# Kernel optimization log

Measured on AMD Instinct MI355X. Metric: run time of the kernel, lower is better.

Reference implementation:

```python
import jax, jax.numpy as jnp
import numpy as np

N, L, V = 8192, 50, 50000   # sentences, max words/sentence, vocab
D, H, O = 300, 150, 64      # embed dim, SAGE hidden, SAGE out
THRESH = 0.7
NEG = -1e9


def _sage_pool(h, A, mask, W1s, W1n, b1, W2s, W2n, b2, gw, gb):
    """Two-layer mean-aggregator SAGEConv + GlobalAttentionPooling, vectorized
    over N independent per-sentence graphs.
    h:[N,L,din] node feats, A:[N,L,L] bool adjacency (src u -> dst v), mask:[N,L] valid nodes."""
    Af = A.astype(h.dtype)
    deg = jnp.maximum(Af.sum(axis=1), 1.0)  # in-degree per dst node [N,L]

    def conv(x, Ws, Wn, b):
        m = jnp.einsum('nuv,nud->nvd', Af, x) / deg[..., None]  # mean of in-neighbors
        return x @ Ws + m @ Wn + b  # fc_self(x) + fc_neigh(mean)

    h1 = jax.nn.relu(conv(h, W1s, W1n, b1))
    h2 = conv(h1, W2s, W2n, b2)
    # global attention pooling: softmax(gate) over real nodes of each graph
    gate = jnp.squeeze(h2 @ gw, -1) + gb  # [N,L]
    attn = jax.nn.softmax(jnp.where(mask, gate, NEG), axis=-1)
    return jnp.einsum('nl,nld->nd', attn, h2)  # [N,O]


def setup_inputs() -> dict:
    key = jax.random.key(0)
    ks = jax.random.split(key, 32)
    pos = jnp.arange(L)
    lengths = jax.random.randint(ks[0], (N,), 5, L + 1)
    valid = pos[None, :] < lengths[:, None]  # [N,L] real-word mask (0 = pad)
    words = jax.random.randint(ks[1], (N, L), 1, V) * valid
    syntax_words = jax.random.randint(ks[2], (N, L), 1, V) * valid
    adj = jax.random.uniform(ks[3], (N, L, L)) < 0.08
    syntax_adj = (adj & valid[:, :, None] & valid[:, None, :]).astype(jnp.int32)
    hsg_feature = jax.random.normal(ks[4], (N, O), jnp.float32)

    def lin(k, i, o):
        return jax.random.normal(k, (i, o), jnp.float32) / np.sqrt(i)

    inp = {
        'words': words.astype(jnp.int32),
        'syntax_words': syntax_words.astype(jnp.int32),
        'syntax_adj': syntax_adj,
        'hsg_feature': hsg_feature,
        'embed': jax.random.normal(ks[5], (V, D), jnp.float32) * 0.1,
        'sem_W1s': lin(ks[6], D, H), 'sem_W1n': lin(ks[7], D, H), 'sem_b1': jnp.zeros((H,), jnp.float32),
        'sem_W2s': lin(ks[8], H, O), 'sem_W2n': lin(ks[9], H, O), 'sem_b2': jnp.zeros((O,), jnp.float32),
        'sem_gw': lin(ks[10], O, 1), 'sem_gb': jnp.zeros((1,), jnp.float32),
        'syn_W1s': lin(ks[11], D, H), 'syn_W1n': lin(ks[12], D, H), 'syn_b1': jnp.zeros((H,), jnp.float32),
        'syn_W2s': lin(ks[13], H, O), 'syn_W2n': lin(ks[14], H, O), 'syn_b2': jnp.zeros((O,), jnp.float32),
        'syn_gw': lin(ks[15], O, 1), 'syn_gb': jnp.zeros((1,), jnp.float32),
        'cls_w1': lin(ks[16], 3 * O, 128), 'cls_b1': jnp.zeros((128,), jnp.float32),
        'cls_w2': lin(ks[17], 128, 2), 'cls_b2': jnp.zeros((2,), jnp.float32),
    }
    return inp


def reference(words, syntax_words, syntax_adj, hsg_feature, embed,
              sem_W1s, sem_W1n, sem_b1, sem_W2s, sem_W2n, sem_b2, sem_gw, sem_gb,
              syn_W1s, syn_W1n, syn_b1, syn_W2s, syn_W2n, syn_b2, syn_gw, syn_gb,
              cls_w1, cls_b1, cls_w2, cls_b2):
    # --- semantic graph: per-sentence cosine-similarity thresholding ---
    mask = words > 0
    emb = embed[words]  # [N,L,D] gather
    nrm = emb / jnp.maximum(jnp.linalg.norm(emb, axis=-1, keepdims=True), 1e-8)
    cos = jnp.einsum('nld,nmd->nlm', nrm, nrm)  # [N,L,L]
    semA = (cos > THRESH) & mask[:, :, None] & mask[:, None, :]  # includes self-loops (cos=1)
    sem_feat = _sage_pool(emb, semA, mask,
                          sem_W1s, sem_W1n, sem_b1, sem_W2s, sem_W2n, sem_b2, sem_gw, sem_gb)
    # --- syntax graph: given per-sentence adjacency over its word ids ---
    syn_mask = syntax_words > 0
    syn_emb = embed[syntax_words]
    syn_feat = _sage_pool(syn_emb, syntax_adj.astype(bool), syn_mask,
                          syn_W1s, syn_W1n, syn_b1, syn_W2s, syn_W2n, syn_b2, syn_gw, syn_gb)
    # --- concat with HSG sentence state, classify ---
    feat = jnp.concatenate([sem_feat, syn_feat, hsg_feature], axis=-1)  # [N,192]
    hid = jax.nn.relu(feat @ cls_w1 + cls_b1)
    return hid @ cls_w2 + cls_b2  # [N,2]
```

## Files before the change

kernel.cpp:

```cpp
#include <hip/hip_runtime.h>

#define NS 8192
#define L  50

typedef unsigned short u16;
typedef unsigned int   u32;
typedef __attribute__((ext_vector_type(8))) __bf16 bf16x8;
typedef __attribute__((ext_vector_type(4))) float  f32x4;

#define OFF_X    0
#define OFF_TT   0
#define OFF_T2T  0
#define OFF_ATTN 0
#define OFF_H1   21760
#define OFF_RED  21760
#define OFF_M    43264
#define OFF_DIAG 43264
#define OFF_WID  52480
#define OFF_CLO  52736
#define OFF_CHI  52992
#define OFF_RDEG 53248
#define SMEM_SZ  53504

#define XSTR  328
#define TSTR  68
#define H1STR 168
#define MSTR  72

#define W1_ROWS 320
#define W1_KP   328
#define W2_ROWS 128
#define W2_KP   168

__device__ __forceinline__ u16 f2bf(float f) {
  u32 u = __float_as_uint(f);
  u += 0x7fffu + ((u >> 16) & 1u);
  return (u16)(u >> 16);
}
__device__ __forceinline__ float bf2f(u16 h) {
  return __uint_as_float(((u32)h) << 16);
}
__device__ __forceinline__ f32x4 mfma16(bf16x8 a, bf16x8 b, f32x4 c) {
  return __builtin_amdgcn_mfma_f32_16x16x32_bf16(a, b, c, 0, 0, 0);
}
__device__ __forceinline__ uint2 pack4bf(f32x4 c) {
  uint2 p;
  p.x = (u32)f2bf(c[0]) | ((u32)f2bf(c[1]) << 16);
  p.y = (u32)f2bf(c[2]) | ((u32)f2bf(c[3]) << 16);
  return p;
}
union BF8U { bf16x8 v; uint4 u; };
__device__ __forceinline__ bf16x8 ld_bf8_b64pair(const u16* p) {
  uint2 a = *(const uint2*)p;
  uint2 b = *(const uint2*)(p + 4);
  BF8U r; r.u = make_uint4(a.x, a.y, b.x, b.y);
  return r.v;
}

struct GParams {
  const int* words; const int* syn_words; const int* syn_adj;
  const float* embed;
  const float* sem_b1; const float* sem_b2; const float* sem_gw; const float* sem_gb;
  const float* syn_b1; const float* syn_b2; const float* syn_gw; const float* syn_gb;
  const u16* w1t_sem; const u16* w1t_syn; const u16* w2t_sem; const u16* w2t_syn;
  float* semf; float* synf;
};

__global__ __launch_bounds__(256, 3) void sage_kernel(GParams P) {
  __shared__ __align__(16) char smem[SMEM_SZ];
  int*   wid   = (int*)(smem + OFF_WID);
  u32*   clo   = (u32*)(smem + OFF_CLO);
  u32*   chi   = (u32*)(smem + OFF_CHI);
  float* rdegp = (float*)(smem + OFF_RDEG);
  float* diag  = (float*)(smem + OFF_DIAG);

  const int tid  = threadIdx.x;
  const int lane = tid & 63;
  const int w    = tid >> 6;
  const int ln   = lane & 15;
  const int quad = lane >> 4;

  const bool semg = (blockIdx.x < NS);
  const int  n    = semg ? blockIdx.x : (blockIdx.x - NS);

  const int*   wsrc = semg ? P.words   : P.syn_words;
  const u16*   W1T  = semg ? P.w1t_sem : P.w1t_syn;
  const u16*   W2T  = semg ? P.w2t_sem : P.w2t_syn;
  const float* b1g  = semg ? P.sem_b1  : P.syn_b1;
  const float* b2g  = semg ? P.sem_b2  : P.syn_b2;
  const float* gw   = semg ? P.sem_gw  : P.syn_gw;
  const float* gb   = semg ? P.sem_gb  : P.syn_gb;
  float* featout    = semg ? P.semf    : P.synf;

  const int jts[3] = {w, w + 4, 8 + (w & 1)};

  if (tid < 64) {
    wid[tid] = (tid < L) ? wsrc[(size_t)n * L + tid] : 0;
    clo[tid] = 0u; chi[tid] = 0u;
  }
  __syncthreads();

  for (int i = 0; i < 16; ++i) {
    const int v = w + 4 * i;
    const int word = wid[v];
    const float* src = P.embed + (size_t)word * 300;
    u16* xrow = (u16*)(smem + OFF_X) + v * XSTR;
    for (int l = lane; l < 82; l += 64) {
      uint2 pk = make_uint2(0u, 0u);
      if (word > 0 && l < 75) {
        float4 f = *(const float4*)(src + l * 4);
        pk.x = (u32)f2bf(f.x) | ((u32)f2bf(f.y) << 16);
        pk.y = (u32)f2bf(f.z) | ((u32)f2bf(f.w) << 16);
      }
      *(uint2*)(xrow + l * 4) = pk;
    }
  }
  __syncthreads();

  if (semg) {
    const f32x4 z4 = {0.f, 0.f, 0.f, 0.f};
    f32x4 g[4] = {z4, z4, z4, z4};
    const char* xb = smem + OFF_X;
    const int arow = (w * 16 + ln) * (XSTR * 2) + quad * 16;
    for (int kk = 0; kk < 10; ++kk) {
      bf16x8 a = *(const bf16x8*)(xb + arow + kk * 64);
      #pragma unroll
      for (int nt = 0; nt < 4; ++nt) {
        bf16x8 b = *(const bf16x8*)(xb + (nt * 16 + ln) * (XSTR * 2) + quad * 16 + kk * 64);
        g[nt] = mfma16(a, b, g[nt]);
      }
    }
    {
      const int r = ln - quad * 4;
      if (r >= 0 && r < 4) {
        #pragma unroll
        for (int nt = 0; nt < 4; ++nt) {
          if (nt == w) {
            float val = (r == 0) ? g[nt][0] : (r == 1) ? g[nt][1]
                      : (r == 2) ? g[nt][2] : g[nt][3];
            diag[w * 16 + ln] = val;
          }
        }
      }
    }
    __syncthreads();
    if (tid < 64) { float dd = diag[tid]; diag[tid] = 1.0f / sqrtf(fmaxf(dd, 1e-12f)); }
    __syncthreads();
    {
      const int ubase = w * 16 + quad * 4;
      float ru[4]; int uok[4];
      #pragma unroll
      for (int r = 0; r < 4; ++r) { ru[r] = diag[ubase + r]; uok[r] = wid[ubase + r] > 0; }
      #pragma unroll
      for (int nt = 0; nt < 4; ++nt) {
        const int v = nt * 16 + ln;
        const float rv = diag[v];
        const bool vok = wid[v] > 0;
        u32 nib = 0u;
        #pragma unroll
        for (int r = 0; r < 4; ++r) {
          float c = g[nt][r] * ru[r] * rv;
          if (vok && uok[r] && c > 0.7f) nib |= (1u << r);
        }
        if (nib) {
          if (ubase < 32) atomicOr(&clo[v], nib << ubase);
          else            atomicOr(&chi[v], nib << (ubase - 32));
        }
      }
    }
  } else {
    const int* abase = P.syn_adj + (size_t)n * (L * L);
    for (int v = w; v < L; v += 4) {
      int val = (lane < L) ? abase[lane * L + v] : 0;
      unsigned long long m = __ballot(val != 0);
      if (lane == 0) { clo[v] = (u32)m; chi[v] = (u32)(m >> 32); }
    }
  }
  __syncthreads();

  if (tid < 64) {
    int dg = __popc(clo[tid]) + __popc(chi[tid]);
    rdegp[tid] = 1.0f / (float)(dg > 0 ? dg : 1);
  }
  {
    const int v = lane, half = w;
    const u32 src = (half < 2) ? clo[v] : chi[v];
    const int sh = (half & 1) * 16;
    u16* Mrow = (u16*)(smem + OFF_M) + v * MSTR + half * 16;
    #pragma unroll
    for (int c = 0; c < 4; ++c) {
      uint2 pk;
      u32 b0 = (src >> (sh + 4 * c + 0)) & 1u;
      u32 b1 = (src >> (sh + 4 * c + 1)) & 1u;
      u32 b2 = (src >> (sh + 4 * c + 2)) & 1u;
      u32 b3 = (src >> (sh + 4 * c + 3)) & 1u;
      pk.x = (b0 ? 0x3F80u : 0u) | (b1 ? 0x3F800000u : 0u);
      pk.y = (b2 ? 0x3F80u : 0u) | (b3 ? 0x3F800000u : 0u);
      *(uint2*)(Mrow + 4 * c) = pk;
    }
  }

  const f32x4 z4 = {0.f, 0.f, 0.f, 0.f};
  f32x4 tacc[3][4], sacc[3][4];
  #pragma unroll
  for (int i = 0; i < 3; ++i)
    #pragma unroll
    for (int m = 0; m < 4; ++m) { tacc[i][m] = z4; sacc[i][m] = z4; }
  {
    const char* xb = smem + OFF_X;
    for (int kk = 0; kk < 10; ++kk) {
      bf16x8 x[4];
      #pragma unroll
      for (int m = 0; m < 4; ++m)
        x[m] = *(const bf16x8*)(xb + (m * 16 + ln) * (XSTR * 2) + quad * 16 + kk * 64);
      bf16x8 bn[3], as[3];
      #pragma unroll
      for (int i = 0; i < 3; ++i) {
        const int jt = jts[i];
        bn[i] = *(const bf16x8*)(W1T + (size_t)(jt * 16 + ln) * W1_KP + kk * 32 + quad * 8);
        as[i] = *(const bf16x8*)(W1T + (size_t)((jt + 10) * 16 + ln) * W1_KP + kk * 32 + quad * 8);
      }
      #pragma unroll
      for (int i = 0; i < 3; ++i)
        #pragma unroll
        for (int m = 0; m < 4; ++m) {
          tacc[i][m] = mfma16(x[m], bn[i], tacc[i][m]);
          sacc[i][m] = mfma16(as[i], x[m], sacc[i][m]);
        }
    }
  }
  __syncthreads();

  {
    u16* tt = (u16*)(smem + OFF_TT);
    #pragma unroll
    for (int i = 0; i < 3; ++i) {
      const int jt = jts[i];
      #pragma unroll
      for (int m = 0; m < 4; ++m) {
        const int v0 = m * 16 + quad * 4;
        *(uint2*)(tt + (jt * 16 + ln) * TSTR + v0) = pack4bf(tacc[i][m]);
      }
    }
  }

  bf16x8 mb0[4], mb1[4];
  {
    const u16* Mp = (const u16*)(smem + OFF_M);
    #pragma unroll
    for (int vt = 0; vt < 4; ++vt) {
      mb0[vt] = *(const bf16x8*)(Mp + (vt * 16 + ln) * MSTR + quad * 8);
      mb1[vt] = *(const bf16x8*)(Mp + (vt * 16 + ln) * MSTR + quad * 8 + 32);
    }
  }
  float rd[4];
  #pragma unroll
  for (int vt = 0; vt < 4; ++vt) rd[vt] = rdegp[vt * 16 + ln];
  {
    const u16* tt = (const u16*)(smem + OFF_TT);
    u16* h1p = (u16*)(smem + OFF_H1);
    #pragma unroll
    for (int i = 0; i < 3; ++i) {
      const int jt = jts[i];
      f32x4 gacc[4] = {z4, z4, z4, z4};
      const u16* tb = tt + (jt * 16 + ln) * TSTR + quad * 8;
      bf16x8 ta0 = ld_bf8_b64pair(tb);
      bf16x8 ta1 = ld_bf8_b64pair(tb + 32);
      #pragma unroll
      for (int vt = 0; vt < 4; ++vt) {
        gacc[vt] = mfma16(ta0, mb0[vt], gacc[vt]);
        gacc[vt] = mfma16(ta1, mb1[vt], gacc[vt]);
      }
      const int j0 = jt * 16 + quad * 4;
      float bv[4];
      #pragma unroll
      for (int r = 0; r < 4; ++r) { int j = j0 + r; bv[r] = (j < 150) ? b1g[j] : 0.f; }
      #pragma unroll
      for (int vt = 0; vt < 4; ++vt) {
        const int v = vt * 16 + ln;
        f32x4 hv;
        #pragma unroll
        for (int r = 0; r < 4; ++r)
          hv[r] = fmaxf(sacc[i][vt][r] + gacc[vt][r] * rd[vt] + bv[r], 0.f);
        *(uint2*)(h1p + v * H1STR + j0) = pack4bf(hv);
      }
    }
  }
  __syncthreads();

  f32x4 s2acc[4] = {z4, z4, z4, z4};
  f32x4 h2v[4];
  {
    f32x4 t2acc[4] = {z4, z4, z4, z4};
    const u16* h1p = (const u16*)(smem + OFF_H1);
    for (int kk = 0; kk < 5; ++kk) {
      bf16x8 h[4];
      #pragma unroll
      for (int t4 = 0; t4 < 4; ++t4)
        h[t4] = *(const bf16x8*)(h1p + (t4 * 16 + ln) * H1STR + kk * 32 + quad * 8);
      bf16x8 a2  = *(const bf16x8*)(W2T + (size_t)(w * 16 + ln) * W2_KP + kk * 32 + quad * 8);
      bf16x8 b2f = *(const bf16x8*)(W2T + (size_t)((4 + w) * 16 + ln) * W2_KP + kk * 32 + quad * 8);
      #pragma unroll
      for (int vt = 0; vt < 4; ++vt) {
        s2acc[vt] = mfma16(a2, h[vt], s2acc[vt]);
        t2acc[vt] = mfma16(h[vt], b2f, t2acc[vt]);
      }
    }
    u16* t2t = (u16*)(smem + OFF_T2T);
    #pragma unroll
    for (int m = 0; m < 4; ++m) {
      const int v0 = m * 16 + quad * 4;
      *(uint2*)(t2t + (w * 16 + ln) * TSTR + v0) = pack4bf(t2acc[m]);
    }
    f32x4 g2[4] = {z4, z4, z4, z4};
    const u16* t2b = t2t + (w * 16 + ln) * TSTR + quad * 8;
    bf16x8 u0 = ld_bf8_b64pair(t2b);
    bf16x8 u1 = ld_bf8_b64pair(t2b + 32);
    #pragma unroll
    for (int vt = 0; vt < 4; ++vt) {
      g2[vt] = mfma16(u0, mb0[vt], g2[vt]);
      g2[vt] = mfma16(u1, mb1[vt], g2[vt]);
    }
    const int j0q = w * 16 + quad * 4;
    float b2v[4];
    #pragma unroll
    for (int r = 0; r < 4; ++r) b2v[r] = b2g[j0q + r];
    #pragma unroll
    for (int vt = 0; vt < 4; ++vt)
      #pragma unroll
      for (int r = 0; r < 4; ++r)
        h2v[vt][r] = s2acc[vt][r] + g2[vt][r] * rd[vt] + b2v[r];
  }
  __syncthreads();

  {
    const int j0q = w * 16 + quad * 4;
    float gwv[4];
    #pragma unroll
    for (int r = 0; r < 4; ++r) gwv[r] = gw[j0q + r];
    float* redp = (float*)(smem + OFF_RED);
    #pragma unroll
    for (int vt = 0; vt < 4; ++vt) {
      float p = h2v[vt][0] * gwv[0] + h2v[vt][1] * gwv[1]
              + h2v[vt][2] * gwv[2] + h2v[vt][3] * gwv[3];
      redp[(vt * 16 + ln) * 17 + (w * 4 + quad)] = p;
    }
  }
  __syncthreads();

  if (tid < 64) {
    const float* redp = (const float*)(smem + OFF_RED);
    float g = gb[0];
    #pragma unroll
    for (int i = 0; i < 16; ++i) g += redp[tid * 17 + i];
    const bool val = wid[tid] > 0;
    g = val ? g : -1e30f;
    float mx = g;
    #pragma unroll
    for (int off = 32; off; off >>= 1) mx = fmaxf(mx, __shfl_xor(mx, off));
    float e = val ? __expf(g - mx) : 0.f;
    float ssum = e;
    #pragma unroll
    for (int off = 32; off; off >>= 1) ssum += __shfl_xor(ssum, off);
    ((float*)(smem + OFF_ATTN))[tid] = e / ssum;
  }
  __syncthreads();

  {
    const float* attnp = (const float*)(smem + OFF_ATTN);
    float av[4];
    #pragma unroll
    for (int vt = 0; vt < 4; ++vt) av[vt] = attnp[vt * 16 + ln];
    float xr[4];
    #pragma unroll
    for (int r = 0; r < 4; ++r) {
      float x = av[0] * h2v[0][r] + av[1] * h2v[1][r]
              + av[2] * h2v[2][r] + av[3] * h2v[3][r];
      #pragma unroll
      for (int off = 1; off < 16; off <<= 1) x += __shfl_xor(x, off);
      xr[r] = x;
    }
    if (ln == 0) {
      const int j0q = w * 16 + quad * 4;
      *(float4*)(featout + (size_t)n * 64 + j0q) = make_float4(xr[0], xr[1], xr[2], xr[3]);
    }
  }
}

__global__ void prep_w1(const float* Wn, const float* Ws, u16* dst) {
  int idx = blockIdx.x * 256 + threadIdx.x;
  if (idx >= W1_ROWS * W1_KP) return;
  int nn = idx / W1_KP, k = idx - nn * W1_KP;
  float v = 0.f;
  if (k < 300) {
    if (nn < 150) v = Wn[k * 150 + nn];
    else if (nn >= 160 && nn < 310) v = Ws[k * 150 + (nn - 160)];
  }
  dst[idx] = f2bf(v);
}
__global__ void prep_w2(const float* Ws, const float* Wn, u16* dst) {
  int idx = blockIdx.x * 256 + threadIdx.x;
  if (idx >= W2_ROWS * W2_KP) return;
  int nn = idx / W2_KP, k = idx - nn * W2_KP;
  float v = 0.f;
  if (k < 150) v = (nn < 64) ? Ws[k * 64 + nn] : Wn[k * 64 + (nn - 64)];
  dst[idx] = f2bf(v);
}

__global__ __launch_bounds__(128) void cls_kernel(const float* semf, const float* synf,
                                                  const float* hsg,
                                                  const float* w1, const float* b1,
                                                  const float* w2, const float* b2,
                                                  float* out) {
  __shared__ float feat[32][192];
  __shared__ float hid[32][132];
  const int r0 = blockIdx.x * 32;
  for (int idx = threadIdx.x; idx < 32 * 192; idx += 128) {
    int r = idx / 192, c = idx % 192;
    float v;
    if (c < 64)        v = semf[(size_t)(r0 + r) * 64 + c];
    else if (c < 128)  v = synf[(size_t)(r0 + r) * 64 + (c - 64)];
    else               v = hsg [(size_t)(r0 + r) * 64 + (c - 128)];
    feat[r][c] = v;
  }
  __syncthreads();
  {
    const int j = threadIdx.x;
    float acc[32];
    float bb = b1[j];
    #pragma unroll
    for (int r = 0; r < 32; ++r) acc[r] = bb;
    for (int k = 0; k < 192; ++k) {
      float ww = w1[(size_t)k * 128 + j];
      #pragma unroll
      for (int r = 0; r < 32; ++r) acc[r] += feat[r][k] * ww;
    }
    #pragma unroll
    for (int r = 0; r < 32; ++r) hid[r][j] = fmaxf(acc[r], 0.0f);
  }
  __syncthreads();
  if (threadIdx.x < 64) {
    const int r = threadIdx.x >> 1, o = threadIdx.x & 1;
    float a = b2[o];
    for (int h = 0; h < 128; ++h) a += hid[r][h] * w2[h * 2 + o];
    out[(size_t)(r0 + r) * 2 + o] = a;
  }
}

extern "C" void kernel_launch(void* const* d_in, const int* in_sizes, int n_in,
                              void* d_out, int out_size, void* d_ws, size_t ws_size,
                              hipStream_t stream) {
  GParams P;
  P.words     = (const int*)d_in[0];
  P.syn_words = (const int*)d_in[1];
  P.syn_adj   = (const int*)d_in[2];
  const float* hsg = (const float*)d_in[3];
  P.embed   = (const float*)d_in[4];
  const float* sem_W1s = (const float*)d_in[5];
  const float* sem_W1n = (const float*)d_in[6];
  P.sem_b1  = (const float*)d_in[7];
  const float* sem_W2s = (const float*)d_in[8];
  const float* sem_W2n = (const float*)d_in[9];
  P.sem_b2  = (const float*)d_in[10];
  P.sem_gw  = (const float*)d_in[11];
  P.sem_gb  = (const float*)d_in[12];
  const float* syn_W1s = (const float*)d_in[13];
  const float* syn_W1n = (const float*)d_in[14];
  P.syn_b1  = (const float*)d_in[15];
  const float* syn_W2s = (const float*)d_in[16];
  const float* syn_W2n = (const float*)d_in[17];
  P.syn_b2  = (const float*)d_in[18];
  P.syn_gw  = (const float*)d_in[19];
  P.syn_gb  = (const float*)d_in[20];
  const float* cls_w1 = (const float*)d_in[21];
  const float* cls_b1 = (const float*)d_in[22];
  const float* cls_w2 = (const float*)d_in[23];
  const float* cls_b2 = (const float*)d_in[24];

  float* semf = (float*)d_ws;
  float* synf = semf + (size_t)NS * 64;
  u16* w1t_sem = (u16*)((char*)d_ws + (size_t)4 * 1024 * 1024);
  u16* w1t_syn = w1t_sem + W1_ROWS * W1_KP;
  u16* w2t_sem = w1t_syn + W1_ROWS * W1_KP;
  u16* w2t_syn = w2t_sem + W2_ROWS * W2_KP;
  P.semf = semf; P.synf = synf;
  P.w1t_sem = w1t_sem; P.w1t_syn = w1t_syn;
  P.w2t_sem = w2t_sem; P.w2t_syn = w2t_syn;

  const int g1 = (W1_ROWS * W1_KP + 255) / 256;
  const int g2 = (W2_ROWS * W2_KP + 255) / 256;
  prep_w1<<<g1, 256, 0, stream>>>(sem_W1n, sem_W1s, w1t_sem);
  prep_w1<<<g1, 256, 0, stream>>>(syn_W1n, syn_W1s, w1t_syn);
  prep_w2<<<g2, 256, 0, stream>>>(sem_W2s, sem_W2n, w2t_sem);
  prep_w2<<<g2, 256, 0, stream>>>(syn_W2s, syn_W2n, w2t_syn);

  sage_kernel<<<2 * NS, 256, 0, stream>>>(P);
  cls_kernel<<<NS / 32, 128, 0, stream>>>(semf, synf, hsg, cls_w1, cls_b1,
                                          cls_w2, cls_b2, (float*)d_out);
}
```

Before: 882.9 us.

## Rebalance layer-1 MFMA work across waves, interleave graph blocks, cheaper bf16 conversion

Several changes at once. Layer-1 output tiles are redistributed so each wave holds 5 accumulator sets instead of 6, and the mask fragments are reloaded from LDS rather than held in registers, cutting register pressure. Semantic and syntax blocks are interleaved by block index. The syntax adjacency is read with coalesced int4 loads plus LDS atomics instead of strided ballots. The embedding bf16 conversion switches to round-half-up without ties-to-even, and the cosine Gram loop reuses B fragments as the A operand. It also adds a barrier before the layer-1 aggregation.

```diff
diff --git a/kernel.cpp b/kernel.cpp
--- a/kernel.cpp
+++ b/kernel.cpp
@@ -37,9 +37,6 @@
   u += 0x7fffu + ((u >> 16) & 1u);
   return (u16)(u >> 16);
 }
-__device__ __forceinline__ float bf2f(u16 h) {
-  return __uint_as_float(((u32)h) << 16);
-}
 __device__ __forceinline__ f32x4 mfma16(bf16x8 a, bf16x8 b, f32x4 c) {
   return __builtin_amdgcn_mfma_f32_16x16x32_bf16(a, b, c, 0, 0, 0);
 }
@@ -80,8 +77,8 @@
   const int ln   = lane & 15;
   const int quad = lane >> 4;
 
-  const bool semg = (blockIdx.x < NS);
-  const int  n    = semg ? blockIdx.x : (blockIdx.x - NS);
+  const bool semg = (blockIdx.x & 1) == 0;
+  const int  n    = blockIdx.x >> 1;
 
   const int*   wsrc = semg ? P.words   : P.syn_words;
   const u16*   W1T  = semg ? P.w1t_sem : P.w1t_syn;
@@ -91,8 +88,6 @@
   const float* gw   = semg ? P.sem_gw  : P.syn_gw;
   const float* gb   = semg ? P.sem_gb  : P.syn_gb;
   float* featout    = semg ? P.semf    : P.synf;
-
-  const int jts[3] = {w, w + 4, 8 + (w & 1)};
 
   if (tid < 64) {
     wid[tid] = (tid < L) ? wsrc[(size_t)n * L + tid] : 0;
@@ -109,8 +104,12 @@
       uint2 pk = make_uint2(0u, 0u);
       if (word > 0 && l < 75) {
         float4 f = *(const float4*)(src + l * 4);
-        pk.x = (u32)f2bf(f.x) | ((u32)f2bf(f.y) << 16);
-        pk.y = (u32)f2bf(f.z) | ((u32)f2bf(f.w) << 16);
+        u32 ax = __float_as_uint(f.x) + 0x8000u;
+        u32 ay = __float_as_uint(f.y) + 0x8000u;
+        u32 az = __float_as_uint(f.z) + 0x8000u;
+        u32 aw = __float_as_uint(f.w) + 0x8000u;
+        pk.x = (ax >> 16) | (ay & 0xffff0000u);
+        pk.y = (az >> 16) | (aw & 0xffff0000u);
       }
       *(uint2*)(xrow + l * 4) = pk;
     }
@@ -121,14 +120,14 @@
     const f32x4 z4 = {0.f, 0.f, 0.f, 0.f};
     f32x4 g[4] = {z4, z4, z4, z4};
     const char* xb = smem + OFF_X;
-    const int arow = (w * 16 + ln) * (XSTR * 2) + quad * 16;
     for (int kk = 0; kk < 10; ++kk) {
-      bf16x8 a = *(const bf16x8*)(xb + arow + kk * 64);
-      #pragma unroll
-      for (int nt = 0; nt < 4; ++nt) {
-        bf16x8 b = *(const bf16x8*)(xb + (nt * 16 + ln) * (XSTR * 2) + quad * 16 + kk * 64);
-        g[nt] = mfma16(a, b, g[nt]);
-      }
+      bf16x8 bfr[4];
+      #pragma unroll
+      for (int nt = 0; nt < 4; ++nt)
+        bfr[nt] = *(const bf16x8*)(xb + (nt * 16 + ln) * (XSTR * 2) + quad * 16 + kk * 64);
+      const bf16x8 a = bfr[w];
+      #pragma unroll
+      for (int nt = 0; nt < 4; ++nt) g[nt] = mfma16(a, bfr[nt], g[nt]);
     }
     {
       const int r = ln - quad * 4;
@@ -170,10 +169,23 @@
     }
   } else {
     const int* abase = P.syn_adj + (size_t)n * (L * L);
-    for (int v = w; v < L; v += 4) {
-      int val = (lane < L) ? abase[lane * L + v] : 0;
-      unsigned long long m = __ballot(val != 0);
-      if (lane == 0) { clo[v] = (u32)m; chi[v] = (u32)(m >> 32); }
+    const int4* a4 = (const int4*)abase;
+    for (int i = 0; i < 3; ++i) {
+      int idx4 = tid + 256 * i;
+      if (idx4 < 625) {
+        int4 a = a4[idx4];
+        int base = idx4 * 4;
+        const int av[4] = {a.x, a.y, a.z, a.w};
+        #pragma unroll
+        for (int e = 0; e < 4; ++e) {
+          if (av[e] != 0) {
+            int el = base + e;
+            int u = el / 50, v = el - u * 50;
+            if (u < 32) atomicOr(&clo[v], 1u << u);
+            else        atomicOr(&chi[v], 1u << (u - 32));
+          }
+        }
+      }
     }
   }
   __syncthreads();
@@ -201,32 +213,43 @@
   }
 
   const f32x4 z4 = {0.f, 0.f, 0.f, 0.f};
-  f32x4 tacc[3][4], sacc[3][4];
+  const int r0w = (w)      * 16 + ln;
+  const int r1w = (w + 4)  * 16 + ln;
+  const int r2w = ((w < 2) ? (w + 8) : (16 + w)) * 16 + ln;
+  const int r3w = (10 + w) * 16 + ln;
+  const int r4w = (14 + w) * 16 + ln;
+  f32x4 acc[5][4];
   #pragma unroll
-  for (int i = 0; i < 3; ++i)
-    #pragma unroll
-    for (int m = 0; m < 4; ++m) { tacc[i][m] = z4; sacc[i][m] = z4; }
+  for (int i = 0; i < 5; ++i)
+    #pragma unroll
+    for (int m = 0; m < 4; ++m) acc[i][m] = z4;
   {
     const char* xb = smem + OFF_X;
     for (int kk = 0; kk < 10; ++kk) {
+      const int wo = kk * 32 + quad * 8;
       bf16x8 x[4];
       #pragma unroll
       for (int m = 0; m < 4; ++m)
         x[m] = *(const bf16x8*)(xb + (m * 16 + ln) * (XSTR * 2) + quad * 16 + kk * 64);
-      bf16x8 bn[3], as[3];
-      #pragma unroll
-      for (int i = 0; i < 3; ++i) {
-        const int jt = jts[i];
-        bn[i] = *(const bf16x8*)(W1T + (size_t)(jt * 16 + ln) * W1_KP + kk * 32 + quad * 8);
-        as[i] = *(const bf16x8*)(W1T + (size_t)((jt + 10) * 16 + ln) * W1_KP + kk * 32 + quad * 8);
-      }
-      #pragma unroll
-      for (int i = 0; i < 3; ++i)
+      bf16x8 bf0 = *(const bf16x8*)(W1T + (size_t)r0w * W1_KP + wo);
+      bf16x8 bf1 = *(const bf16x8*)(W1T + (size_t)r1w * W1_KP + wo);
+      bf16x8 bf2 = *(const bf16x8*)(W1T + (size_t)r2w * W1_KP + wo);
+      bf16x8 bf3 = *(const bf16x8*)(W1T + (size_t)r3w * W1_KP + wo);
+      bf16x8 bf4 = *(const bf16x8*)(W1T + (size_t)r4w * W1_KP + wo);
+      #pragma unroll
+      for (int m = 0; m < 4; ++m) {
+        acc[0][m] = mfma16(x[m], bf0, acc[0][m]);
+        acc[1][m] = mfma16(x[m], bf1, acc[1][m]);
+        acc[3][m] = mfma16(bf3, x[m], acc[3][m]);
+        acc[4][m] = mfma16(bf4, x[m], acc[4][m]);
+      }
+      if (w < 2) {
         #pragma unroll
-        for (int m = 0; m < 4; ++m) {
-          tacc[i][m] = mfma16(x[m], bn[i], tacc[i][m]);
-          sacc[i][m] = mfma16(as[i], x[m], sacc[i][m]);
-        }
+        for (int m = 0; m < 4; ++m) acc[2][m] = mfma16(x[m], bf2, acc[2][m]);
+      } else {
+        #pragma unroll
+        for (int m = 0; m < 4; ++m) acc[2][m] = mfma16(bf2, x[m], acc[2][m]);
+      }
     }
   }
   __syncthreads();
@@ -234,36 +257,37 @@
   {
     u16* tt = (u16*)(smem + OFF_TT);
     #pragma unroll
-    for (int i = 0; i < 3; ++i) {
-      const int jt = jts[i];
+    for (int m = 0; m < 4; ++m) {
+      const int v0 = m * 16 + quad * 4;
+      *(uint2*)(tt + ((w)     * 16 + ln) * TSTR + v0) = pack4bf(acc[0][m]);
+      *(uint2*)(tt + ((w + 4) * 16 + ln) * TSTR + v0) = pack4bf(acc[1][m]);
+    }
+    if (w < 2) {
       #pragma unroll
       for (int m = 0; m < 4; ++m) {
         const int v0 = m * 16 + quad * 4;
-        *(uint2*)(tt + (jt * 16 + ln) * TSTR + v0) = pack4bf(tacc[i][m]);
-      }
-    }
-  }
-
-  bf16x8 mb0[4], mb1[4];
-  {
+        *(uint2*)(tt + ((w + 8) * 16 + ln) * TSTR + v0) = pack4bf(acc[2][m]);
+      }
+    }
+  }
+  __syncthreads();
+
+  float rd[4];
+  #pragma unroll
+  for (int vt = 0; vt < 4; ++vt) rd[vt] = rdegp[vt * 16 + ln];
+  {
+    const u16* tt = (const u16*)(smem + OFF_TT);
     const u16* Mp = (const u16*)(smem + OFF_M);
+    bf16x8 mb0[4], mb1[4];
     #pragma unroll
     for (int vt = 0; vt < 4; ++vt) {
       mb0[vt] = *(const bf16x8*)(Mp + (vt * 16 + ln) * MSTR + quad * 8);
       mb1[vt] = *(const bf16x8*)(Mp + (vt * 16 + ln) * MSTR + quad * 8 + 32);
     }
-  }
-  float rd[4];
-  #pragma unroll
-  for (int vt = 0; vt < 4; ++vt) rd[vt] = rdegp[vt * 16 + ln];
-  {
-    const u16* tt = (const u16*)(smem + OFF_TT);
     u16* h1p = (u16*)(smem + OFF_H1);
-    #pragma unroll
-    for (int i = 0; i < 3; ++i) {
-      const int jt = jts[i];
+    auto slot = [&](f32x4 (&sac)[4], int g) {
       f32x4 gacc[4] = {z4, z4, z4, z4};
-      const u16* tb = tt + (jt * 16 + ln) * TSTR + quad * 8;
+      const u16* tb = tt + (g * 16 + ln) * TSTR + quad * 8;
       bf16x8 ta0 = ld_bf8_b64pair(tb);
       bf16x8 ta1 = ld_bf8_b64pair(tb + 32);
       #pragma unroll
@@ -271,7 +295,7 @@
         gacc[vt] = mfma16(ta0, mb0[vt], gacc[vt]);
         gacc[vt] = mfma16(ta1, mb1[vt], gacc[vt]);
       }
-      const int j0 = jt * 16 + quad * 4;
+      const int j0 = g * 16 + quad * 4;
       float bv[4];
       #pragma unroll
       for (int r = 0; r < 4; ++r) { int j = j0 + r; bv[r] = (j < 150) ? b1g[j] : 0.f; }
@@ -281,25 +305,29 @@
         f32x4 hv;
         #pragma unroll
         for (int r = 0; r < 4; ++r)
-          hv[r] = fmaxf(sacc[i][vt][r] + gacc[vt][r] * rd[vt] + bv[r], 0.f);
+          hv[r] = fmaxf(sac[vt][r] + gacc[vt][r] * rd[vt] + bv[r], 0.f);
         *(uint2*)(h1p + v * H1STR + j0) = pack4bf(hv);
       }
-    }
-  }
-  __syncthreads();
-
-  f32x4 s2acc[4] = {z4, z4, z4, z4};
+    };
+    if (w >= 2) slot(acc[2], w + 6);
+    slot(acc[3], w);
+    slot(acc[4], w + 4);
+  }
+  __syncthreads();
+
   f32x4 h2v[4];
   {
+    f32x4 s2acc[4] = {z4, z4, z4, z4};
     f32x4 t2acc[4] = {z4, z4, z4, z4};
     const u16* h1p = (const u16*)(smem + OFF_H1);
     for (int kk = 0; kk < 5; ++kk) {
+      const int wo = kk * 32 + quad * 8;
       bf16x8 h[4];
       #pragma unroll
       for (int t4 = 0; t4 < 4; ++t4)
-        h[t4] = *(const bf16x8*)(h1p + (t4 * 16 + ln) * H1STR + kk * 32 + quad * 8);
-      bf16x8 a2  = *(const bf16x8*)(W2T + (size_t)(w * 16 + ln) * W2_KP + kk * 32 + quad * 8);
-      bf16x8 b2f = *(const bf16x8*)(W2T + (size_t)((4 + w) * 16 + ln) * W2_KP + kk * 32 + quad * 8);
+        h[t4] = *(const bf16x8*)(h1p + (t4 * 16 + ln) * H1STR + wo);
+      bf16x8 a2  = *(const bf16x8*)(W2T + (size_t)(w * 16 + ln) * W2_KP + wo);
+      bf16x8 b2f = *(const bf16x8*)(W2T + (size_t)((4 + w) * 16 + ln) * W2_KP + wo);
       #pragma unroll
       for (int vt = 0; vt < 4; ++vt) {
         s2acc[vt] = mfma16(a2, h[vt], s2acc[vt]);
@@ -312,14 +340,17 @@
       const int v0 = m * 16 + quad * 4;
       *(uint2*)(t2t + (w * 16 + ln) * TSTR + v0) = pack4bf(t2acc[m]);
     }
+    const u16* Mp = (const u16*)(smem + OFF_M);
     f32x4 g2[4] = {z4, z4, z4, z4};
     const u16* t2b = t2t + (w * 16 + ln) * TSTR + quad * 8;
     bf16x8 u0 = ld_bf8_b64pair(t2b);
     bf16x8 u1 = ld_bf8_b64pair(t2b + 32);
     #pragma unroll
     for (int vt = 0; vt < 4; ++vt) {
-      g2[vt] = mfma16(u0, mb0[vt], g2[vt]);
-      g2[vt] = mfma16(u1, mb1[vt], g2[vt]);
+      bf16x8 m0 = *(const bf16x8*)(Mp + (vt * 16 + ln) * MSTR + quad * 8);
+      bf16x8 m1 = *(const bf16x8*)(Mp + (vt * 16 + ln) * MSTR + quad * 8 + 32);
+      g2[vt] = mfma16(u0, m0, g2[vt]);
+      g2[vt] = mfma16(u1, m1, g2[vt]);
     }
     const int j0q = w * 16 + quad * 4;
     float b2v[4];
```

Measured after the change: 2.017 ms. 2.28x slower.

## Restructure SAGE kernel: fused gram+W1 loop, role-split waves, merged prep launches

Applied to the files above, without the earlier changes.

The embedding gather is rewritten so each lane loads a row chunk with wider 16-byte stores, using a cheaper round-half-up bf16 conversion. The cosine Gram matmul is folded into the layer-1 K loop so the X tile is read once. Waves now split roles: two compute the neighbour-transform tiles and two the self tiles, with five tiles each. The softmax result moves through register shuffles instead of shared memory, dropping a barrier, and the four weight-prep launches become one. Risks are higher register pressure from 20 accumulators, uneven work between the two wave roles, and slightly different bf16 rounding on ties.

```diff
diff --git a/kernel.cpp b/kernel.cpp
--- a/kernel.cpp
+++ b/kernel.cpp
@@ -11,9 +11,8 @@
 #define OFF_X    0
 #define OFF_TT   0
 #define OFF_T2T  0
-#define OFF_ATTN 0
+#define OFF_RED  9216
 #define OFF_H1   21760
-#define OFF_RED  21760
 #define OFF_M    43264
 #define OFF_DIAG 43264
 #define OFF_WID  52480
@@ -26,19 +25,19 @@
 #define TSTR  68
 #define H1STR 168
 #define MSTR  72
+#define RSTR  20
 
 #define W1_ROWS 320
 #define W1_KP   328
 #define W2_ROWS 128
 #define W2_KP   168
+#define W1SZ (W1_ROWS * W1_KP)
+#define W2SZ (W2_ROWS * W2_KP)
 
 __device__ __forceinline__ u16 f2bf(float f) {
   u32 u = __float_as_uint(f);
   u += 0x7fffu + ((u >> 16) & 1u);
   return (u16)(u >> 16);
-}
-__device__ __forceinline__ float bf2f(u16 h) {
-  return __uint_as_float(((u32)h) << 16);
 }
 __device__ __forceinline__ f32x4 mfma16(bf16x8 a, bf16x8 b, f32x4 c) {
   return __builtin_amdgcn_mfma_f32_16x16x32_bf16(a, b, c, 0, 0, 0);
@@ -92,88 +91,152 @@
   const float* gb   = semg ? P.sem_gb  : P.syn_gb;
   float* featout    = semg ? P.semf    : P.synf;
 
-  const int jts[3] = {w, w + 4, 8 + (w & 1)};
-
-  if (tid < 64) {
-    wid[tid] = (tid < L) ? wsrc[(size_t)n * L + tid] : 0;
-    clo[tid] = 0u; chi[tid] = 0u;
-  }
-  __syncthreads();
-
-  for (int i = 0; i < 16; ++i) {
-    const int v = w + 4 * i;
-    const int word = wid[v];
+  {
+    const int r    = w * 16 + (lane >> 2);
+    const int part = lane & 3;
+    int word = 0;
+    if (r < L) word = wsrc[(size_t)n * L + r];
     const float* src = P.embed + (size_t)word * 300;
-    u16* xrow = (u16*)(smem + OFF_X) + v * XSTR;
-    for (int l = lane; l < 82; l += 64) {
-      uint2 pk = make_uint2(0u, 0u);
-      if (word > 0 && l < 75) {
-        float4 f = *(const float4*)(src + l * 4);
-        pk.x = (u32)f2bf(f.x) | ((u32)f2bf(f.y) << 16);
-        pk.y = (u32)f2bf(f.z) | ((u32)f2bf(f.w) << 16);
-      }
-      *(uint2*)(xrow + l * 4) = pk;
-    }
-  }
-  __syncthreads();
-
-  if (semg) {
-    const f32x4 z4 = {0.f, 0.f, 0.f, 0.f};
-    f32x4 g[4] = {z4, z4, z4, z4};
-    const char* xb = smem + OFF_X;
-    const int arow = (w * 16 + ln) * (XSTR * 2) + quad * 16;
-    for (int kk = 0; kk < 10; ++kk) {
-      bf16x8 a = *(const bf16x8*)(xb + arow + kk * 64);
-      #pragma unroll
-      for (int nt = 0; nt < 4; ++nt) {
-        bf16x8 b = *(const bf16x8*)(xb + (nt * 16 + ln) * (XSTR * 2) + quad * 16 + kk * 64);
-        g[nt] = mfma16(a, b, g[nt]);
-      }
-    }
-    {
-      const int r = ln - quad * 4;
-      if (r >= 0 && r < 4) {
-        #pragma unroll
-        for (int nt = 0; nt < 4; ++nt) {
-          if (nt == w) {
-            float val = (r == 0) ? g[nt][0] : (r == 1) ? g[nt][1]
-                      : (r == 2) ? g[nt][2] : g[nt][3];
-            diag[w * 16 + ln] = val;
+    u16* xrow = (u16*)(smem + OFF_X) + r * XSTR;
+    #pragma unroll
+    for (int k = 0; k < 11; ++k) {
+      const int s = part + 4 * k;
+      if (s < 41) {
+        uint4 out = make_uint4(0u, 0u, 0u, 0u);
+        if (word > 0) {
+          const int e = s * 8;
+          if (e < 300) {
+            float4 f = *(const float4*)(src + e);
+            u32 ax = __float_as_uint(f.x) + 0x8000u;
+            u32 ay = __float_as_uint(f.y) + 0x8000u;
+            u32 az = __float_as_uint(f.z) + 0x8000u;
+            u32 aw = __float_as_uint(f.w) + 0x8000u;
+            out.x = (ax >> 16) | (ay & 0xffff0000u);
+            out.y = (az >> 16) | (aw & 0xffff0000u);
+          }
+          if (e + 4 < 300) {
+            float4 f = *(const float4*)(src + e + 4);
+            u32 ax = __float_as_uint(f.x) + 0x8000u;
+            u32 ay = __float_as_uint(f.y) + 0x8000u;
+            u32 az = __float_as_uint(f.z) + 0x8000u;
+            u32 aw = __float_as_uint(f.w) + 0x8000u;
+            out.z = (ax >> 16) | (ay & 0xffff0000u);
+            out.w = (az >> 16) | (aw & 0xffff0000u);
           }
         }
-      }
-    }
-    __syncthreads();
-    if (tid < 64) { float dd = diag[tid]; diag[tid] = 1.0f / sqrtf(fmaxf(dd, 1e-12f)); }
-    __syncthreads();
-    {
-      const int ubase = w * 16 + quad * 4;
-      float ru[4]; int uok[4];
-      #pragma unroll
-      for (int r = 0; r < 4; ++r) { ru[r] = diag[ubase + r]; uok[r] = wid[ubase + r] > 0; }
-      #pragma unroll
-      for (int nt = 0; nt < 4; ++nt) {
-        const int v = nt * 16 + ln;
-        const float rv = diag[v];
-        const bool vok = wid[v] > 0;
-        u32 nib = 0u;
-        #pragma unroll
-        for (int r = 0; r < 4; ++r) {
-          float c = g[nt][r] * ru[r] * rv;
-          if (vok && uok[r] && c > 0.7f) nib |= (1u << r);
-        }
-        if (nib) {
-          if (ubase < 32) atomicOr(&clo[v], nib << ubase);
-          else            atomicOr(&chi[v], nib << (ubase - 32));
-        }
-      }
-    }
-  } else {
+        *(uint4*)(xrow + s * 8) = out;
+      }
+    }
+    if (tid < 64) {
+      wid[tid] = (tid < L) ? wsrc[(size_t)n * L + tid] : 0;
+      clo[tid] = 0u; chi[tid] = 0u;
+    }
+  }
+  __syncthreads();
+
+  const f32x4 z4 = {0.f, 0.f, 0.f, 0.f};
+
+  if (!semg) {
     const int* abase = P.syn_adj + (size_t)n * (L * L);
     for (int v = w; v < L; v += 4) {
       int val = (lane < L) ? abase[lane * L + v] : 0;
       unsigned long long m = __ballot(val != 0);
       if (lane == 0) { clo[v] = (u32)m; chi[v] = (u32)(m >> 32); }
+    }
+  }
+
+  f32x4 acc[5][4];
+  f32x4 g[4] = {z4, z4, z4, z4};
+  #pragma unroll
+  for (int i = 0; i < 5; ++i)
+    #pragma unroll
+    for (int m = 0; m < 4; ++m) acc[i][m] = z4;
+  {
+    const char* xb = smem + OFF_X;
+    const u16* W1p[5];
+    #pragma unroll
+    for (int i = 0; i < 5; ++i) {
+      const int base = (w < 2) ? (w * 5 + i) : (10 + (w - 2) * 5 + i);
+      W1p[i] = W1T + (size_t)(base * 16 + ln) * W1_KP + quad * 8;
+    }
+    const int arow = (w * 16 + ln) * (XSTR * 2) + quad * 16;
+    for (int kk = 0; kk < 10; ++kk) {
+      const int xo = quad * 16 + kk * 64;
+      bf16x8 x[4];
+      #pragma unroll
+      for (int m = 0; m < 4; ++m)
+        x[m] = *(const bf16x8*)(xb + (m * 16 + ln) * (XSTR * 2) + xo);
+      bf16x8 bw[5];
+      #pragma unroll
+      for (int i = 0; i < 5; ++i) bw[i] = *(const bf16x8*)(W1p[i] + kk * 32);
+      if (semg) {
+        bf16x8 a = *(const bf16x8*)(xb + arow + kk * 64);
+        #pragma unroll
+        for (int nt = 0; nt < 4; ++nt) g[nt] = mfma16(a, x[nt], g[nt]);
+      }
+      if (w < 2) {
+        #pragma unroll
+        for (int i = 0; i < 5; ++i)
+          #pragma unroll
+          for (int m = 0; m < 4; ++m) acc[i][m] = mfma16(x[m], bw[i], acc[i][m]);
+      } else {
+        #pragma unroll
+        for (int i = 0; i < 5; ++i)
+          #pragma unroll
+          for (int m = 0; m < 4; ++m) acc[i][m] = mfma16(bw[i], x[m], acc[i][m]);
+      }
+    }
+  }
+  if (semg) {
+    const int r = ln - quad * 4;
+    if (r >= 0 && r < 4) {
+      #pragma unroll
+      for (int nt = 0; nt < 4; ++nt) {
+        if (nt == w) {
+          float val = (r == 0) ? g[nt][0] : (r == 1) ? g[nt][1]
+                    : (r == 2) ? g[nt][2] : g[nt][3];
+          diag[w * 16 + ln] = val;
+        }
+      }
+    }
+  }
+  __syncthreads();
+
+  if (semg) {
+    const int ubase = w * 16 + quad * 4;
+    float ru[4]; int uok[4];
+    #pragma unroll
+    for (int r = 0; r < 4; ++r) {
+      ru[r] = rsqrtf(fmaxf(diag[ubase + r], 1e-12f));
+      uok[r] = wid[ubase + r] > 0;
+    }
+    #pragma unroll
+    for (int nt = 0; nt < 4; ++nt) {
+      const int v = nt * 16 + ln;
+      const float rv = rsqrtf(fmaxf(diag[v], 1e-12f));
+      const bool vok = wid[v] > 0;
+      u32 nib = 0u;
+      #pragma unroll
+      for (int r = 0; r < 4; ++r) {
+        float c = g[nt][r] * ru[r] * rv;
+        if (vok && uok[r] && c > 0.7f) nib |= (1u << r);
+      }
+      if (nib) {
+        if (ubase < 32) atomicOr(&clo[v], nib << ubase);
+        else            atomicOr(&chi[v], nib << (ubase - 32));
+      }
+    }
+  }
+  if (w < 2) {
+    u16* tt = (u16*)(smem + OFF_TT);
+    #pragma unroll
+    for (int i = 0; i < 5; ++i) {
+      const int gg = w * 5 + i;
+      #pragma unroll
+      for (int m = 0; m < 4; ++m) {
+        const int v0 = m * 16 + quad * 4;
+        *(uint2*)(tt + (gg * 16 + ln) * TSTR + v0) = pack4bf(acc[i][m]);
+      }
     }
   }
   __syncthreads();
@@ -199,50 +262,11 @@
       *(uint2*)(Mrow + 4 * c) = pk;
     }
   }
-
-  const f32x4 z4 = {0.f, 0.f, 0.f, 0.f};
-  f32x4 tacc[3][4], sacc[3][4];
+  __syncthreads();
+
+  float rd[4];
   #pragma unroll
-  for (int i = 0; i < 3; ++i)
-    #pragma unroll
-    for (int m = 0; m < 4; ++m) { tacc[i][m] = z4; sacc[i][m] = z4; }
-  {
-    const char* xb = smem + OFF_X;
-    for (int kk = 0; kk < 10; ++kk) {
-      bf16x8 x[4];
-      #pragma unroll
-      for (int m = 0; m < 4; ++m)
-        x[m] = *(const bf16x8*)(xb + (m * 16 + ln) * (XSTR * 2) + quad * 16 + kk * 64);
-      bf16x8 bn[3], as[3];
-      #pragma unroll
-      for (int i = 0; i < 3; ++i) {
-        const int jt = jts[i];
-        bn[i] = *(const bf16x8*)(W1T + (size_t)(jt * 16 + ln) * W1_KP + kk * 32 + quad * 8);
-        as[i] = *(const bf16x8*)(W1T + (size_t)((jt + 10) * 16 + ln) * W1_KP + kk * 32 + quad * 8);
-      }
-      #pragma unroll
-      for (int i = 0; i < 3; ++i)
-        #pragma unroll
-        for (int m = 0; m < 4; ++m) {
-          tacc[i][m] = mfma16(x[m], bn[i], tacc[i][m]);
-          sacc[i][m] = mfma16(as[i], x[m], sacc[i][m]);
-        }
-    }
-  }
-  __syncthreads();
-
-  {
-    u16* tt = (u16*)(smem + OFF_TT);
-    #pragma unroll
-    for (int i = 0; i < 3; ++i) {
-      const int jt = jts[i];
-      #pragma unroll
-      for (int m = 0; m < 4; ++m) {
-        const int v0 = m * 16 + quad * 4;
-        *(uint2*)(tt + (jt * 16 + ln) * TSTR + v0) = pack4bf(tacc[i][m]);
-      }
-    }
-  }
+  for (int vt = 0; vt < 4; ++vt) rd[vt] = rdegp[vt * 16 + ln];
 
   bf16x8 mb0[4], mb1[4];
   {
@@ -253,25 +277,23 @@
       mb1[vt] = *(const bf16x8*)(Mp + (vt * 16 + ln) * MSTR + quad * 8 + 32);
     }
   }
-  float rd[4];
-  #pragma unroll
-  for (int vt = 0; vt < 4; ++vt) rd[vt] = rdegp[vt * 16 + ln];
-  {
+
+  if (w >= 2) {
     const u16* tt = (const u16*)(smem + OFF_TT);
     u16* h1p = (u16*)(smem + OFF_H1);
     #pragma unroll
-    for (int i = 0; i < 3; ++i) {
-      const int jt = jts[i];
-      f32x4 gacc[4] = {z4, z4, z4, z4};
-      const u16* tb = tt + (jt * 16 + ln) * TSTR + quad * 8;
+    for (int i = 0; i < 5; ++i) {
+      const int gg = (w - 2) * 5 + i;
+      const u16* tb = tt + (gg * 16 + ln) * TSTR + quad * 8;
       bf16x8 ta0 = ld_bf8_b64pair(tb);
       bf16x8 ta1 = ld_bf8_b64pair(tb + 32);
+      f32x4 gacc[4] = {z4, z4, z4, z4};
       #pragma unroll
       for (int vt = 0; vt < 4; ++vt) {
         gacc[vt] = mfma16(ta0, mb0[vt], gacc[vt]);
         gacc[vt] = mfma16(ta1, mb1[vt], gacc[vt]);
       }
-      const int j0 = jt * 16 + quad * 4;
+      const int j0 = gg * 16 + quad * 4;
       float bv[4];
       #pragma unroll
       for (int r = 0; r < 4; ++r) { int j = j0 + r; bv[r] = (j < 150) ? b1g[j] : 0.f; }
@@ -281,25 +303,26 @@
         f32x4 hv;
         #pragma unroll
         for (int r = 0; r < 4; ++r)
-          hv[r] = fmaxf(sacc[i][vt][r] + gacc[vt][r] * rd[vt] + bv[r], 0.f);
+          hv[r] = fmaxf(acc[i][vt][r] + gacc[vt][r] * rd[vt] + bv[r], 0.f);
         *(uint2*)(h1p + v * H1STR + j0) = pack4bf(hv);
       }
     }
   }
   __syncthreads();
 
-  f32x4 s2acc[4] = {z4, z4, z4, z4};
   f32x4 h2v[4];
   {
+    f32x4 s2acc[4] = {z4, z4, z4, z4};
     f32x4 t2acc[4] = {z4, z4, z4, z4};
     const u16* h1p = (const u16*)(smem + OFF_H1);
     for (int kk = 0; kk < 5; ++kk) {
+      const int wo = kk * 32 + quad * 8;
       bf16x8 h[4];
       #pragma unroll
       for (int t4 = 0; t4 < 4; ++t4)
-        h[t4] = *(const bf16x8*)(h1p + (t4 * 16 + ln) * H1STR + kk * 32 + quad * 8);
-      bf16x8 a2  = *(const bf16x8*)(W2T + (size_t)(w * 16 + ln) * W2_KP + kk * 32 + quad * 8);
-      bf16x8 b2f = *(const bf16x8*)(W2T + (size_t)((4 + w) * 16 + ln) * W2_KP + kk * 32 + quad * 8);
+        h[t4] = *(const bf16x8*)(h1p + (t4 * 16 + ln) * H1STR + wo);
+      bf16x8 a2  = *(const bf16x8*)(W2T + (size_t)(w * 16 + ln) * W2_KP + wo);
+      bf16x8 b2f = *(const bf16x8*)(W2T + (size_t)((4 + w) * 16 + ln) * W2_KP + wo);
       #pragma unroll
       for (int vt = 0; vt < 4; ++vt) {
         s2acc[vt] = mfma16(a2, h[vt], s2acc[vt]);
@@ -343,17 +366,21 @@
     for (int vt = 0; vt < 4; ++vt) {
       float p = h2v[vt][0] * gwv[0] + h2v[vt][1] * gwv[1]
               + h2v[vt][2] * gwv[2] + h2v[vt][3] * gwv[3];
-      redp[(vt * 16 + ln) * 17 + (w * 4 + quad)] = p;
-    }
-  }
-  __syncthreads();
-
-  if (tid < 64) {
-    const float* redp = (const float*)(smem + OFF_RED);
-    float g = gb[0];
-    #pragma unroll
-    for (int i = 0; i < 16; ++i) g += redp[tid * 17 + i];
-    const bool val = wid[tid] > 0;
+      redp[(vt * 16 + ln) * RSTR + (w * 4 + quad)] = p;
+    }
+  }
+  __syncthreads();
+
+  float attnv;
+  {
+    const float* redp = (const float*)(smem + OFF_RED) + lane * RSTR;
+    f32x4 r0 = *(const f32x4*)(redp);
+    f32x4 r1 = *(const f32x4*)(redp + 4);
+    f32x4 r2 = *(const f32x4*)(redp + 8);
+    f32x4 r3 = *(const f32x4*)(redp + 12);
+    float g = gb[0] + r0[0] + r0[1] + r0[2] + r0[3] + r1[0] + r1[1] + r1[2] + r1[3]
+            + r2[0] + r2[1] + r2[2] + r2[3] + r3[0] + r3[1] + r3[2] + r3[3];
+    const bool val = wid[lane] > 0;
     g = val ? g : -1e30f;
     float mx = g;
     #pragma unroll
@@ -362,15 +389,13 @@
     float ssum = e;
     #pragma unroll
     for (int off = 32; off; off >>= 1) ssum += __shfl_xor(ssum, off);
-    ((float*)(smem + OFF_ATTN))[tid] = e / ssum;
-  }
-  __syncthreads();
-
-  {
-    const float* attnp = (const float*)(smem + OFF_ATTN);
+    attnv = e / ssum;
+  }
+
+  {
     float av[4];
     #pragma unroll
-    for (int vt = 0; vt < 4; ++vt) av[vt] = attnp[vt * 16 + ln];
+    for (int vt = 0; vt < 4; ++vt) av[vt] = __shfl(attnv, vt * 16 + ln);
     float xr[4];
     #pragma unroll
     for (int r = 0; r < 4; ++r) {
@@ -387,24 +412,37 @@
   }
 }
 
-__global__ void prep_w1(const float* Wn, const float* Ws, u16* dst) {
+__global__ void prep_all(const float* sem_W1n, const float* sem_W1s,
+                         const float* syn_W1n, const float* syn_W1s,
+                         const float* sem_W2s, const float* sem_W2n,
+                         const float* syn_W2s, const float* syn_W2n,
+                         u16* w1t_sem, u16* w1t_syn, u16* w2t_sem, u16* w2t_syn) {
   int idx = blockIdx.x * 256 + threadIdx.x;
-  if (idx >= W1_ROWS * W1_KP) return;
-  int nn = idx / W1_KP, k = idx - nn * W1_KP;
-  float v = 0.f;
-  if (k < 300) {
-    if (nn < 150) v = Wn[k * 150 + nn];
-    else if (nn >= 160 && nn < 310) v = Ws[k * 150 + (nn - 160)];
-  }
-  dst[idx] = f2bf(v);
-}
-__global__ void prep_w2(const float* Ws, const float* Wn, u16* dst) {
-  int idx = blockIdx.x * 256 + threadIdx.x;
-  if (idx >= W2_ROWS * W2_KP) return;
-  int nn = idx / W2_KP, k = idx - nn * W2_KP;
-  float v = 0.f;
-  if (k < 150) v = (nn < 64) ? Ws[k * 64 + nn] : Wn[k * 64 + (nn - 64)];
-  dst[idx] = f2bf(v);
+  if (idx < 2 * W1SZ) {
+    const bool sem = idx < W1SZ;
+    const int li = sem ? idx : idx - W1SZ;
+    const float* Wn = sem ? sem_W1n : syn_W1n;
+    const float* Ws = sem ? sem_W1s : syn_W1s;
+    u16* dst = sem ? w1t_sem : w1t_syn;
+    int nn = li / W1_KP, k = li - nn * W1_KP;
+    float v = 0.f;
+    if (k < 300) {
+      if (nn < 150) v = Wn[k * 150 + nn];
+      else if (nn >= 160 && nn < 310) v = Ws[k * 150 + (nn - 160)];
+    }
+    dst[li] = f2bf(v);
+  } else if (idx < 2 * W1SZ + 2 * W2SZ) {
+    int j = idx - 2 * W1SZ;
+    const bool sem = j < W2SZ;
+    const int li = sem ? j : j - W2SZ;
+    const float* Ws = sem ? sem_W2s : syn_W2s;
+    const float* Wn = sem ? sem_W2n : syn_W2n;
+    u16* dst = sem ? w2t_sem : w2t_syn;
+    int nn = li / W2_KP, k = li - nn * W2_KP;
+    float v = 0.f;
+    if (k < 150) v = (nn < 64) ? Ws[k * 64 + nn] : Wn[k * 64 + (nn - 64)];
+    dst[li] = f2bf(v);
+  }
 }
 
 __global__ __launch_bounds__(128) void cls_kernel(const float* semf, const float* synf,
@@ -480,19 +518,18 @@
   float* semf = (float*)d_ws;
   float* synf = semf + (size_t)NS * 64;
   u16* w1t_sem = (u16*)((char*)d_ws + (size_t)4 * 1024 * 1024);
-  u16* w1t_syn = w1t_sem + W1_ROWS * W1_KP;
-  u16* w2t_sem = w1t_syn + W1_ROWS * W1_KP;
-  u16* w2t_syn = w2t_sem + W2_ROWS * W2_KP;
+  u16* w1t_syn = w1t_sem + W1SZ;
+  u16* w2t_sem = w1t_syn + W1SZ;
+  u16* w2t_syn = w2t_sem + W2SZ;
   P.semf = semf; P.synf = synf;
   P.w1t_sem = w1t_sem; P.w1t_syn = w1t_syn;
   P.w2t_sem = w2t_sem; P.w2t_syn = w2t_syn;
 
-  const int g1 = (W1_ROWS * W1_KP + 255) / 256;
-  const int g2 = (W2_ROWS * W2_KP + 255) / 256;
-  prep_w1<<<g1, 256, 0, stream>>>(sem_W1n, sem_W1s, w1t_sem);
-  prep_w1<<<g1, 256, 0, stream>>>(syn_W1n, syn_W1s, w1t_syn);
-  prep_w2<<<g2, 256, 0, stream>>>(sem_W2s, sem_W2n, w2t_sem);
-  prep_w2<<<g2, 256, 0, stream>>>(syn_W2s, syn_W2n, w2t_syn);
+  const int total = 2 * W1SZ + 2 * W2SZ;
+  prep_all<<<(total + 255) / 256, 256, 0, stream>>>(
+      sem_W1n, sem_W1s, syn_W1n, syn_W1s,
+      sem_W2s, sem_W2n, syn_W2s, syn_W2n,
+      w1t_sem, w1t_syn, w2t_sem, w2t_syn);
 
   sage_kernel<<<2 * NS, 256, 0, stream>>>(P);
   cls_kernel<<<NS / 32, 128, 0, stream>>>(semf, synf, hsg, cls_w1, cls_b1,
```

Measured after the change: 2.058 ms. 2.33x slower.
